# Kernel tuning notes

Measured on AMD Instinct MI355X. Metric: run time of the kernel, lower is better.

## Reference

```python
import jax, jax.numpy as jnp
import numpy as np

# sRGB -> XYZ matrix (skimage/CIE, D65 observer 2deg)
_RGB2XYZ = jnp.array([[0.412453, 0.357580, 0.180423],
                      [0.212671, 0.715160, 0.072169],
                      [0.019334, 0.119193, 0.950227]], dtype=jnp.float32)
_WHITE_D65 = jnp.array([0.95047, 1.0, 1.08883], dtype=jnp.float32)


def _srgb_to_linear(c):
    # inverse sRGB gamma
    return jnp.where(c > 0.04045, ((c + 0.055) / 1.055) ** 2.4, c / 12.92)


def _xyz_f(t):
    # CIE Lab nonlinearity
    eps = 0.008856
    return jnp.where(t > eps, jnp.cbrt(t), 7.787 * t + 16.0 / 116.0)


def _rgb2lab(img):
    # img: [..., H, W, 3] sRGB in [0,1]
    lin = _srgb_to_linear(img)
    xyz = jnp.einsum('...c,dc->...d', lin, _RGB2XYZ) / _WHITE_D65
    f = _xyz_f(xyz)
    fx, fy, fz = f[..., 0], f[..., 1], f[..., 2]
    L = 116.0 * fy - 16.0
    a = 500.0 * (fx - fy)
    b = 200.0 * (fy - fz)
    return jnp.stack([L, a, b], axis=-1)


def setup_inputs() -> dict:
    key = jax.random.key(0)
    x = jax.random.uniform(key, (512, 128, 128, 3), dtype=jnp.float32)
    return {"x": x}


def reference(x) -> jnp.ndarray:
    lab = _rgb2lab(x)                       # [B,H,W,3]
    L = lab[..., 0]
    # per-image min-max normalize L channel (reduce over H,W)
    Lmin = jnp.min(L, axis=(1, 2), keepdims=True)
    Lmax = jnp.max(L, axis=(1, 2), keepdims=True)
    L01 = (L - Lmin) / (Lmax - Lmin)
    ab01 = (lab[..., 1:] + 128.0) / 255.0
    out = jnp.concatenate([L01[..., None], ab01], axis=-1)
    return jax.lax.stop_gradient(out).astype(jnp.float32)
```

## Files before the change

### kernel.cpp

```cpp
#include <hip/hip_runtime.h>

typedef unsigned int uint32;

__device__ __forceinline__ float fexp2(float x) { return __builtin_amdgcn_exp2f(x); }
__device__ __forceinline__ float flog2(float x) { return __builtin_amdgcn_logf(x); }

__device__ __forceinline__ float s2lin(float c) {
    float p = fexp2(flog2((c + 0.055f) * (1.0f / 1.055f)) * 2.4f);
    return c > 0.04045f ? p : c * (1.0f / 12.92f);
}

__device__ __forceinline__ float labf(float t) {
    float p = fexp2(flog2(t) * (1.0f / 3.0f));
    return t > 0.008856f ? p : 7.787f * t + (16.0f / 116.0f);
}

__device__ __forceinline__ void px(float r, float g, float b,
                                   float& L, float& a01, float& b01) {
    float lr = s2lin(r), lg = s2lin(g), lb = s2lin(b);
    float X = 0.43395300f * lr + 0.37621900f * lg + 0.18982460f * lb;
    float Y = 0.21267100f * lr + 0.71516000f * lg + 0.07216900f * lb;
    float Z = 0.01775660f * lr + 0.10946970f * lg + 0.87270740f * lb;
    float fx = labf(X), fy = labf(Y), fz = labf(Z);
    L   = 116.0f * fy - 16.0f;
    a01 = (500.0f * (fx - fy) + 128.0f) * (1.0f / 255.0f);
    b01 = (200.0f * (fy - fz) + 128.0f) * (1.0f / 255.0f);
}

__global__ __launch_bounds__(1024) void k_fused(const float* __restrict__ x,
                                                float* __restrict__ out) {
    const int img = blockIdx.x, t = threadIdx.x;
    const size_t base = (size_t)img * 49152;
    const float* __restrict__ in = x + base;
    float* __restrict__ o = out + base;

    uint32 pk[16];
    float m1 = 3.4e38f, m2 = 3.4e38f;
#pragma unroll
    for (int i = 0; i < 16; ++i) {
        const int p = t + (i << 10);
        const float* q = in + 3 * p;
        float L, a01, b01;
        px(q[0], q[1], q[2], L, a01, b01);
        m1 = fminf(m1, L);
        m2 = fminf(m2, 100.0f - L);
        uint32 au = (uint32)(a01 * 255.0f + 0.5f);
        uint32 bu = (uint32)(b01 * 255.0f + 0.5f);
        unsigned short hb = __builtin_bit_cast(unsigned short, (_Float16)L);
        pk[i] = au | (bu << 8) | ((uint32)hb << 16);
    }

#pragma unroll
    for (int m = 32; m; m >>= 1) {
        m1 = fminf(m1, __shfl_xor(m1, m, 64));
        m2 = fminf(m2, __shfl_xor(m2, m, 64));
    }
    __shared__ float sm[32];
    if ((t & 63) == 0) { sm[(t >> 6) * 2] = m1; sm[(t >> 6) * 2 + 1] = m2; }
    __syncthreads();
    float Lmin = 3.4e38f, M2 = 3.4e38f;
#pragma unroll
    for (int i = 0; i < 16; ++i) {
        Lmin = fminf(Lmin, sm[2 * i]);
        M2   = fminf(M2,   sm[2 * i + 1]);
    }
    const float s = 1.0f / ((100.0f - M2) - Lmin);

#pragma unroll
    for (int i = 0; i < 16; ++i) {
        const int p = t + (i << 10);
        const uint32 v = pk[i];
        float a01 = (float)(v & 255u) * (1.0f / 255.0f);
        float b01 = (float)((v >> 8) & 255u) * (1.0f / 255.0f);
        float L = (float)__builtin_bit_cast(_Float16, (unsigned short)(v >> 16));
        float* q = o + 3 * p;
        q[0] = (L - Lmin) * s;
        q[1] = a01;
        q[2] = b01;
    }
}

extern "C" void kernel_launch(void* const* d_in, const int* in_sizes, int n_in,
                              void* d_out, int out_size, void* d_ws, size_t ws_size,
                              hipStream_t stream) {
    (void)in_sizes; (void)n_in; (void)out_size; (void)d_ws; (void)ws_size;
    const float* x = (const float*)d_in[0];
    float* out = (float*)d_out;
    k_fused<<<512, 1024, 0, stream>>>(x, out);
}
```

Baseline: 183.7 us.

## Stage input through LDS with async global_load_lds in three-quarter ring

Adds a kernel that copies each image's input into 144 KB of LDS using the global_load_lds builtin (16-byte per lane), in quarters. The fourth quarter's load is issued into the first buffer slot while the second and third quarters are computed. This replaces strided per-thread 12-byte global loads with coalesced bulk DMA into LDS. In exchange, the large LDS allocation limits occupancy to one block per CU, adds extra barriers, and needs a dynamic shared memory attribute; the original kernel is kept as a fallback.

```diff
diff --git a/kernel.cpp b/kernel.cpp
--- a/kernel.cpp
+++ b/kernel.cpp
@@ -27,8 +27,94 @@
     b01 = (200.0f * (fy - fz) + 128.0f) * (1.0f / 255.0f);
 }
 
-__global__ __launch_bounds__(1024) void k_fused(const float* __restrict__ x,
-                                                float* __restrict__ out) {
+__device__ __forceinline__ uint32 packpx(float L, float a01, float b01) {
+    uint32 au = (uint32)(a01 * 255.0f + 0.5f);
+    uint32 bu = (uint32)(b01 * 255.0f + 0.5f);
+    unsigned short hb = __builtin_bit_cast(unsigned short, (_Float16)L);
+    return au | (bu << 8) | ((uint32)hb << 16);
+}
+
+typedef __attribute__((address_space(1))) const void gconst_void;
+typedef __attribute__((address_space(3))) void lds_void;
+
+__device__ __forceinline__ void gload16(const void* g, void* l) {
+    __builtin_amdgcn_global_load_lds((gconst_void*)g, (lds_void*)l, 16, 0, 0);
+}
+
+#define IMG_BYTES 196608
+#define QTR_BYTES 49152
+
+__device__ __forceinline__ void do_quarter(const float* __restrict__ sf, int t, int q,
+                                           uint32* pk, float& m1, float& m2) {
+#pragma unroll
+    for (int i = 0; i < 4; ++i) {
+        const int p = t + (i << 10);
+        float L, a01, b01;
+        px(sf[3 * p], sf[3 * p + 1], sf[3 * p + 2], L, a01, b01);
+        m1 = fminf(m1, L); m2 = fminf(m2, 100.0f - L);
+        pk[(q << 2) + i] = packpx(L, a01, b01);
+    }
+}
+
+__global__ __launch_bounds__(1024) void k_gl(const float* __restrict__ x,
+                                             float* __restrict__ out) {
+    extern __shared__ char stage[];
+    __shared__ float sm[32];
+    const int t = threadIdx.x, img = blockIdx.x;
+    const int wave = t >> 6, lane = t & 63;
+    const char* gimg = (const char*)x + (size_t)img * IMG_BYTES;
+    float* __restrict__ o = out + (size_t)img * 49152;
+
+#pragma unroll
+    for (int q = 0; q < 3; ++q)
+#pragma unroll
+        for (int j = 0; j < 3; ++j)
+            gload16(gimg + q * QTR_BYTES + (wave * 3 + j) * 1024 + lane * 16,
+                    stage + q * QTR_BYTES + (wave * 3 + j) * 1024);
+
+    uint32 pk[16];
+    float m1 = 3.4e38f, m2 = 3.4e38f;
+
+    __syncthreads();
+    do_quarter((const float*)stage, t, 0, pk, m1, m2);
+    __syncthreads();
+#pragma unroll
+    for (int j = 0; j < 3; ++j)
+        gload16(gimg + 3 * QTR_BYTES + (wave * 3 + j) * 1024 + lane * 16,
+                stage + (wave * 3 + j) * 1024);
+    do_quarter((const float*)(stage + QTR_BYTES), t, 1, pk, m1, m2);
+    do_quarter((const float*)(stage + 2 * QTR_BYTES), t, 2, pk, m1, m2);
+    __syncthreads();
+    do_quarter((const float*)stage, t, 3, pk, m1, m2);
+
+#pragma unroll
+    for (int m = 32; m; m >>= 1) {
+        m1 = fminf(m1, __shfl_xor(m1, m, 64));
+        m2 = fminf(m2, __shfl_xor(m2, m, 64));
+    }
+    if ((t & 63) == 0) { sm[(t >> 6) * 2] = m1; sm[(t >> 6) * 2 + 1] = m2; }
+    __syncthreads();
+    float Lmin = 3.4e38f, M2 = 3.4e38f;
+#pragma unroll
+    for (int i = 0; i < 16; ++i) {
+        Lmin = fminf(Lmin, sm[2 * i]);
+        M2   = fminf(M2,   sm[2 * i + 1]);
+    }
+    const float s = 1.0f / ((100.0f - M2) - Lmin);
+
+#pragma unroll
+    for (int k = 0; k < 16; ++k) {
+        const int q = k >> 2, i = k & 3;
+        const uint32 v = pk[k];
+        float* w = o + 3 * ((q << 12) + (i << 10) + t);
+        w[0] = ((float)__builtin_bit_cast(_Float16, (unsigned short)(v >> 16)) - Lmin) * s;
+        w[1] = (float)(v & 255u) * (1.0f / 255.0f);
+        w[2] = (float)((v >> 8) & 255u) * (1.0f / 255.0f);
+    }
+}
+
+__global__ __launch_bounds__(1024) void k_fb(const float* __restrict__ x,
+                                             float* __restrict__ out) {
     const int img = blockIdx.x, t = threadIdx.x;
     const size_t base = (size_t)img * 49152;
     const float* __restrict__ in = x + base;
@@ -44,12 +130,8 @@
         px(q[0], q[1], q[2], L, a01, b01);
         m1 = fminf(m1, L);
         m2 = fminf(m2, 100.0f - L);
-        uint32 au = (uint32)(a01 * 255.0f + 0.5f);
-        uint32 bu = (uint32)(b01 * 255.0f + 0.5f);
-        unsigned short hb = __builtin_bit_cast(unsigned short, (_Float16)L);
-        pk[i] = au | (bu << 8) | ((uint32)hb << 16);
+        pk[i] = packpx(L, a01, b01);
     }
-
 #pragma unroll
     for (int m = 32; m; m >>= 1) {
         m1 = fminf(m1, __shfl_xor(m1, m, 64));
@@ -65,18 +147,14 @@
         M2   = fminf(M2,   sm[2 * i + 1]);
     }
     const float s = 1.0f / ((100.0f - M2) - Lmin);
-
 #pragma unroll
     for (int i = 0; i < 16; ++i) {
         const int p = t + (i << 10);
         const uint32 v = pk[i];
-        float a01 = (float)(v & 255u) * (1.0f / 255.0f);
-        float b01 = (float)((v >> 8) & 255u) * (1.0f / 255.0f);
-        float L = (float)__builtin_bit_cast(_Float16, (unsigned short)(v >> 16));
         float* q = o + 3 * p;
-        q[0] = (L - Lmin) * s;
-        q[1] = a01;
-        q[2] = b01;
+        q[0] = ((float)__builtin_bit_cast(_Float16, (unsigned short)(v >> 16)) - Lmin) * s;
+        q[1] = (float)(v & 255u) * (1.0f / 255.0f);
+        q[2] = (float)((v >> 8) & 255u) * (1.0f / 255.0f);
     }
 }
 
@@ -86,5 +164,16 @@
     (void)in_sizes; (void)n_in; (void)out_size; (void)d_ws; (void)ws_size;
     const float* x = (const float*)d_in[0];
     float* out = (float*)d_out;
-    k_fused<<<512, 1024, 0, stream>>>(x, out);
+
+    static int attr_ok = -1;
+    if (attr_ok < 0) {
+        attr_ok = (hipFuncSetAttribute((const void*)k_gl,
+                                       hipFuncAttributeMaxDynamicSharedMemorySize,
+                                       3 * QTR_BYTES) == hipSuccess) ? 1 : 0;
+    }
+    if (attr_ok) {
+        k_gl<<<512, 1024, 3 * QTR_BYTES, stream>>>(x, out);
+    } else {
+        k_fb<<<512, 1024, 0, stream>>>(x, out);
+    }
 }
```

New measurement: 190.0 us. 1.03x slower.
